# Optimization experiments

Measured on AMD Instinct MI355X. Metric: run time of the kernel, lower is better.

The kernel has to match this reference:

```python
import jax, jax.numpy as jnp
import numpy as np

B, C, H, W = 16, 3, 1024, 1024
OUT_HW = 224  # F.interpolate target size before the ResNet backbone
EPS = 1e-8


def setup_inputs() -> dict:
    key = jax.random.key(0)
    images = jax.random.uniform(key, (B, C, H, W), dtype=jnp.float32)
    return {"images": images}


def reference(images):
    # Batched FFT2 over spatial dims (replaces the per-(b,c) CPU numpy loop)
    fft = jnp.fft.fft2(images, axes=(-2, -1))                 # complex64 (B,C,H,W)
    fft = jnp.fft.fftshift(fft, axes=(-2, -1))
    spec = jnp.log1p(jnp.abs(fft))                             # log-magnitude spectrum

    # Per-sample min/max normalization to [0, 1] (flatten over C,H,W)
    b = spec.shape[0]
    flat = spec.reshape(b, -1)
    mn = flat.min(axis=1).reshape(b, 1, 1, 1)
    mx = flat.max(axis=1).reshape(b, 1, 1, 1)
    spec = (spec - mn) / (mx - mn + EPS)

    # Bilinear resize to 224x224; jax.image.resize 'bilinear' uses half-pixel
    # centers, matching torch F.interpolate(align_corners=False).
    out = jax.image.resize(spec, (b, spec.shape[1], OUT_HW, OUT_HW), method='bilinear')
    return out
```

## Files before the change

### kernel.cpp

```cpp
#include <hip/hip_runtime.h>
#include <math.h>

#define N 1024
#define BATCH 16
#define CH 3
#define BC 48
#define OUTHW 224
#define KSCALE (1024.0f / 224.0f)
#define SCALE  (224.0f / 1024.0f)
#define ABYTES ((size_t)BC * N * N * 8)
#define T1OFF  (768 * 2048)
#define SLOTOFF 1802240
#define WBAR() __builtin_amdgcn_wave_barrier()

#define CMUL(dr, di, ar, ai, br, bi) do {                         \
    float _r = (ar) * (br) - (ai) * (bi);                         \
    float _i = (ar) * (bi) + (ai) * (br);                         \
    (dr) = _r; (di) = _i; } while (0)

#define RADIX4(ar,ai,br,bi,cr,ci,dr,di, o0r,o0i,o1r,o1i,o2r,o2i,o3r,o3i) do { \
    float u0r=(ar)+(cr), u0i=(ai)+(ci);                           \
    float u1r=(ar)-(cr), u1i=(ai)-(ci);                           \
    float u2r=(br)+(dr), u2i=(bi)+(di);                           \
    float u3r=(bi)-(di), u3i=(dr)-(br);                           \
    (o0r)=u0r+u2r; (o0i)=u0i+u2i;                                 \
    (o1r)=u1r+u3r; (o1i)=u1i+u3i;                                 \
    (o2r)=u0r-u2r; (o2i)=u0i-u2i;                                 \
    (o3r)=u1r-u3r; (o3i)=u1i-u3i; } while (0)

__device__ __forceinline__ void dft16(float* xr, float* xi) {
  const float W16R[4][4] = {
    {1.f, 1.f, 1.f, 1.f},
    {1.f,  0.9238795325f,  0.7071067812f,  0.3826834324f},
    {1.f,  0.7071067812f,  0.0f,          -0.7071067812f},
    {1.f,  0.3826834324f, -0.7071067812f, -0.9238795325f}};
  const float W16I[4][4] = {
    {0.f, 0.f, 0.f, 0.f},
    {0.f, -0.3826834324f, -0.7071067812f, -0.9238795325f},
    {0.f, -0.7071067812f, -1.0f,          -0.7071067812f},
    {0.f, -0.9238795325f, -0.7071067812f,  0.3826834324f}};
  float tr[16], ti[16];
#pragma unroll
  for (int j = 0; j < 4; ++j) {
    RADIX4(xr[j],xi[j], xr[j+4],xi[j+4], xr[j+8],xi[j+8], xr[j+12],xi[j+12],
           tr[4*j],ti[4*j], tr[4*j+1],ti[4*j+1], tr[4*j+2],ti[4*j+2], tr[4*j+3],ti[4*j+3]);
  }
#pragma unroll
  for (int j = 0; j < 4; ++j) {
    float ar[4], ai_[4];
#pragma unroll
    for (int k = 0; k < 4; ++k) {
      if (j == 0 || k == 0) { ar[k] = tr[j+4*k]; ai_[k] = ti[j+4*k]; }
      else CMUL(ar[k], ai_[k], tr[j+4*k], ti[j+4*k], W16R[j][k], W16I[j][k]);
    }
    RADIX4(ar[0],ai_[0], ar[1],ai_[1], ar[2],ai_[2], ar[3],ai_[3],
           xr[j],xi[j], xr[j+4],xi[j+4], xr[j+8],xi[j+8], xr[j+12],xi[j+12]);
  }
}

__device__ __forceinline__ void stage2(float* xr, float* xi,
                                       const float2* __restrict__ twg, int j2) {
#pragma unroll
  for (int k = 1; k < 16; ++k) {
    float2 w = twg[4 * j2 * k];
    CMUL(xr[k], xi[k], xr[k], xi[k], w.x, w.y);
  }
  dft16(xr, xi);
}

__device__ __forceinline__ void wave_fft1024(float* xr, float* xi,
                                             float* sre, float* sim,
                                             const float2* __restrict__ twg, int l) {
  dft16(xr, xi);
#pragma unroll
  for (int k = 0; k < 16; ++k) { sre[17*l + k] = xr[k]; sim[17*l + k] = xi[k]; }
  WBAR();
  const int base2 = l + (l >> 4);
#pragma unroll
  for (int k = 0; k < 16; ++k) { xr[k] = sre[base2 + 68*k]; xi[k] = sim[base2 + 68*k]; }
  const int j2 = l & 15;
  stage2(xr, xi, twg, j2);
  const int ob = 272 * (l >> 4) + j2;
#pragma unroll
  for (int k = 0; k < 16; ++k) { sre[ob + 17*k] = xr[k]; sim[ob + 17*k] = xi[k]; }
  WBAR();
#pragma unroll
  for (int m = 0; m < 4; ++m) {
    float ar[4], ai_[4];
#pragma unroll
    for (int k = 0; k < 4; ++k) {
      ar[k] = sre[base2 + 68*m + 272*k];
      ai_[k] = sim[base2 + 68*m + 272*k];
    }
    const int j = l + 64*m;
#pragma unroll
    for (int k = 1; k < 4; ++k) {
      float2 w = twg[j * k];
      CMUL(ar[k], ai_[k], ar[k], ai_[k], w.x, w.y);
    }
    RADIX4(ar[0],ai_[0], ar[1],ai_[1], ar[2],ai_[2], ar[3],ai_[3],
           xr[m],xi[m], xr[m+4],xi[m+4], xr[m+8],xi[m+8], xr[m+12],xi[m+12]);
  }
}

__device__ __forceinline__ void wave_fft1024_1buf(float* xr, float* xi,
                                                  float* wb,
                                                  const float2* __restrict__ twg,
                                                  int l) {
  const int base2 = l + (l >> 4);
  const int j2 = l & 15;
  const int ob = 272 * (l >> 4) + j2;
  dft16(xr, xi);
#pragma unroll
  for (int k = 0; k < 16; ++k) wb[17*l + k] = xr[k];
  WBAR();
#pragma unroll
  for (int k = 0; k < 16; ++k) xr[k] = wb[base2 + 68*k];
  WBAR();
#pragma unroll
  for (int k = 0; k < 16; ++k) wb[17*l + k] = xi[k];
  WBAR();
#pragma unroll
  for (int k = 0; k < 16; ++k) xi[k] = wb[base2 + 68*k];
  WBAR();
  stage2(xr, xi, twg, j2);
#pragma unroll
  for (int k = 0; k < 16; ++k) wb[ob + 17*k] = xr[k];
  WBAR();
#pragma unroll
  for (int m = 0; m < 4; ++m)
#pragma unroll
    for (int k = 0; k < 4; ++k) xr[m + 4*k] = wb[base2 + 68*m + 272*k];
  WBAR();
#pragma unroll
  for (int k = 0; k < 16; ++k) wb[ob + 17*k] = xi[k];
  WBAR();
#pragma unroll
  for (int m = 0; m < 4; ++m)
#pragma unroll
    for (int k = 0; k < 4; ++k) xi[m + 4*k] = wb[base2 + 68*m + 272*k];
  WBAR();
#pragma unroll
  for (int m = 0; m < 4; ++m) {
    float ar[4], ai_[4];
#pragma unroll
    for (int k = 0; k < 4; ++k) { ar[k] = xr[m + 4*k]; ai_[k] = xi[m + 4*k]; }
    const int j = l + 64*m;
#pragma unroll
    for (int k = 1; k < 4; ++k) {
      float2 w = twg[j * k];
      CMUL(ar[k], ai_[k], ar[k], ai_[k], w.x, w.y);
    }
    RADIX4(ar[0],ai_[0], ar[1],ai_[1], ar[2],ai_[2], ar[3],ai_[3],
           xr[m],xi[m], xr[m+4],xi[m+4], xr[m+8],xi[m+8], xr[m+12],xi[m+12]);
  }
}

__global__ void k_init(float2* __restrict__ tw, int* __restrict__ slots) {
  int g = blockIdx.x * 256 + threadIdx.x;
  if (g < 1024) {
    float ang = -6.283185307179586f * ((float)g / 1024.0f);
    float s, c;
    sincosf(ang, &s, &c);
    tw[g] = make_float2(c, s);
    slots[g] = 0x7F800000;
  } else {
    slots[g] = 0;
  }
}

__global__ __launch_bounds__(256, 4) void k_rowfft(const float* __restrict__ in,
                                                   float2* __restrict__ A,
                                                   const float2* __restrict__ twg) {
  __shared__ float lds[8704];
  const int t  = threadIdx.x;
  const int w  = t >> 6;
  const int l  = t & 63;
  const int bc  = blockIdx.x >> 7;
  const int h0b = (blockIdx.x & 127) << 3;
  const int r0  = h0b + 2 * w;
  float* sre = lds + w * 2176;
  float* sim = sre + 1088;
  const float* row0 = in + ((size_t)bc << 20) + ((size_t)r0 << 10);
  const float* row1 = row0 + N;
  float xr[16], xi[16];
  const float sgn = (l & 1) ? -1.0f : 1.0f;
#pragma unroll
  for (int k = 0; k < 16; ++k) {
    xr[k] =  sgn * row0[l + 64*k];
    xi[k] = -sgn * row1[l + 64*k];
  }
  wave_fft1024(xr, xi, sre, sim, twg, l);
#pragma unroll
  for (int s = 0; s < 16; ++s) { sre[l + 64*s] = xr[s]; sim[l + 64*s] = xi[s]; }
  WBAR();
  float arr[9], ari[9], brr[9], bri[9];
#pragma unroll
  for (int s = 0; s < 9; ++s) {
    int i  = l + 64*s;
    int nk = (N - i) & (N - 1);
    float pr = xr[s], pi = xi[s];
    float qr = sre[nk], qi = sim[nk];
    arr[s] = 0.5f * (pr + qr); ari[s] = 0.5f * (pi - qi);
    brr[s] = 0.5f * (pi + qi); bri[s] = 0.5f * (qr - pr);
  }
  __syncthreads();
  float* stre = lds;
  float* stim = lds + 4160;
#pragma unroll
  for (int s = 0; s < 9; ++s) {
    int i = l + 64*s;
    if (i <= 512) {
      stre[(2*w)     * 520 + i] = arr[s]; stim[(2*w)     * 520 + i] = ari[s];
      stre[(2*w + 1) * 520 + i] = brr[s]; stim[(2*w + 1) * 520 + i] = bri[s];
    }
  }
  __syncthreads();
  const int rr = t & 7, v0 = t >> 3;
  float2* Abc = A + ((size_t)bc << 20);
#pragma unroll
  for (int i2 = 0; i2 < 17; ++i2) {
    int v = v0 + 32 * i2;
    if (v <= 512) {
      Abc[(size_t)v * N + h0b + rr] = make_float2(stre[rr*520 + v], stim[rr*520 + v]);
    }
  }
}

__global__ __launch_bounds__(256, 8) void k_colfft(const float2* __restrict__ A,
                                                   float* __restrict__ WSf,
                                                   int* __restrict__ slots,
                                                   const float2* __restrict__ twg) {
  __shared__ float lds[4352];
  const int t  = threadIdx.x;
  const int w  = t >> 6;
  const int l  = t & 63;
  const int gw = blockIdx.x * 4 + w;
  const int bc = gw / 513;
  const int sx = gw - bc * 513;
  const int b  = bc / CH;
  float* wb = lds + w * 1088;
  const float2* src = A + ((size_t)bc << 20) + ((size_t)sx << 10);
  float xr[16], xi[16];
#pragma unroll
  for (int k = 0; k < 16; ++k) { float2 v = src[l + 64*k]; xr[k] = v.x; xi[k] = v.y; }
  wave_fft1024_1buf(xr, xi, wb, twg, l);
  float lmin = 3.4e38f, lmax = 0.0f;
#pragma unroll
  for (int s = 0; s < 16; ++s) {
    float sp = __logf(1.0f + sqrtf(xr[s]*xr[s] + xi[s]*xi[s]));
    wb[l + 64*s] = sp;
    lmin = fminf(lmin, sp); lmax = fmaxf(lmax, sp);
  }
#pragma unroll
  for (int off = 32; off; off >>= 1) {
    lmin = fminf(lmin, __shfl_xor(lmin, off));
    lmax = fmaxf(lmax, __shfl_xor(lmax, off));
  }
  if (l == 0) {
    atomicMin(&slots[b * 64 + (sx & 63)],        __float_as_int(lmin));
    atomicMax(&slots[1024 + b * 64 + (sx & 63)], __float_as_int(lmax));
  }
  WBAR();
  float* T1 = WSf + ((size_t)bc << 21) + T1OFF;
  const bool mir = (sx != 0) && (sx != 512);
#pragma unroll
  for (int obk = 0; obk < 4; ++obk) {
    int oh = l + 64 * obk;
    if (oh < OUTHW) {
      float x = ((float)oh + 0.5f) * KSCALE - 0.5f;
      int jlo = (int)ceilf(x - KSCALE);
      float ssum = 0.0f, acc = 0.0f, accm = 0.0f;
#pragma unroll
      for (int u = 0; u < 10; ++u) {
        int j = jlo + u;
        float wgt = 1.0f - fabsf((float)j - x) * SCALE;
        wgt = fmaxf(wgt, 0.0f);
        bool valid = (j >= 0) && (j <= N - 1);
        if (!valid) wgt = 0.0f;
        int ja = valid ? j : 0;
        ssum += wgt;
        acc  += wgt * wb[ja];
        accm += wgt * wb[(N - ja) & (N - 1)];
      }
      float inv = 1.0f / ssum;
      T1[(size_t)sx * OUTHW + oh] = acc * inv;
      if (mir) T1[(size_t)(N - sx) * OUTHW + oh] = accm * inv;
    }
  }
}

__global__ __launch_bounds__(256) void k_resize2(const float2* __restrict__ A,
                                                 const int* __restrict__ slots,
                                                 float* __restrict__ out) {
  __shared__ float s2[2];
  const int ow = blockIdx.x % OUTHW;
  const int bc = blockIdx.x / OUTHW;
  const int b  = bc / CH;
  const int t  = threadIdx.x;
  if (t < 64) {
    int mn = slots[b * 64 + t];
#pragma unroll
    for (int off = 32; off; off >>= 1) mn = min(mn, __shfl_xor(mn, off));
    if (t == 0) s2[0] = __int_as_float(mn);
  } else if (t < 128) {
    int mx = slots[1024 + b * 64 + (t - 64)];
#pragma unroll
    for (int off = 32; off; off >>= 1) mx = max(mx, __shfl_xor(mx, off));
    if (t == 64) s2[1] = __int_as_float(mx);
  }
  __syncthreads();
  if (t >= OUTHW) return;
  const float mn = s2[0];
  const float mx = s2[1];
  const float inv = 1.0f / (mx - mn + 1e-8f);
  const float* T1 = (const float*)(A + ((size_t)bc << 20)) + T1OFF;
  float x = ((float)ow + 0.5f) * KSCALE - 0.5f;
  int jlo = (int)ceilf(x - KSCALE);
  float ssum = 0.0f, acc = 0.0f;
#pragma unroll
  for (int u = 0; u < 10; ++u) {
    int j = jlo + u;
    float wv = 1.0f - fabsf((float)j - x) * SCALE;
    wv = fmaxf(wv, 0.0f);
    bool valid = (j >= 0) && (j <= N - 1);
    if (!valid) wv = 0.0f;
    int ja = valid ? j : 0;
    ssum += wv;
    acc += wv * T1[(size_t)ja * OUTHW + t];
  }
  float v = acc / ssum;
  out[((size_t)bc * OUTHW + t) * OUTHW + ow] = (v - mn) * inv;
}

extern "C" void kernel_launch(void* const* d_in, const int* in_sizes, int n_in,
                              void* d_out, int out_size, void* d_ws, size_t ws_size,
                              hipStream_t stream) {
  const float* in = (const float*)d_in[0];
  float* out = (float*)d_out;
  float2* A = (float2*)d_ws;
  float* WSf = (float*)d_ws;
  float2* twg = (float2*)((char*)d_ws + ABYTES + 128);
  int* slots = (int*)(WSf + SLOTOFF);

  k_init<<<8, 256, 0, stream>>>(twg, slots);
  k_rowfft<<<BC * 128, 256, 0, stream>>>(in, A, twg);
  k_colfft<<<(BC * 513) / 4, 256, 0, stream>>>(A, WSf, slots, twg);
  k_resize2<<<BC * OUTHW, 256, 0, stream>>>(A, slots, out);
}
```

Baseline: 431.2 us.

## Widen row-FFT blocks to 16 rows with single-buffer LDS and split transposed store

The row-FFT kernel now runs 512-thread blocks that each handle 16 rows instead of 8. It switches to the single-buffer wave FFT, which stages real and imaginary parts through one LDS buffer per wave. The real/complex split and the transposed staging are done in two halves of the spectrum so that 16 rows fit in the same LDS. The goal is longer contiguous runs in the transposed global writes (16 consecutive complex values per column) and better occupancy. The cost is extra LDS round trips and barriers for the split passes.

```diff
diff --git a/kernel.cpp b/kernel.cpp
--- a/kernel.cpp
+++ b/kernel.cpp
@@ -68,41 +68,6 @@
   dft16(xr, xi);
 }
 
-__device__ __forceinline__ void wave_fft1024(float* xr, float* xi,
-                                             float* sre, float* sim,
-                                             const float2* __restrict__ twg, int l) {
-  dft16(xr, xi);
-#pragma unroll
-  for (int k = 0; k < 16; ++k) { sre[17*l + k] = xr[k]; sim[17*l + k] = xi[k]; }
-  WBAR();
-  const int base2 = l + (l >> 4);
-#pragma unroll
-  for (int k = 0; k < 16; ++k) { xr[k] = sre[base2 + 68*k]; xi[k] = sim[base2 + 68*k]; }
-  const int j2 = l & 15;
-  stage2(xr, xi, twg, j2);
-  const int ob = 272 * (l >> 4) + j2;
-#pragma unroll
-  for (int k = 0; k < 16; ++k) { sre[ob + 17*k] = xr[k]; sim[ob + 17*k] = xi[k]; }
-  WBAR();
-#pragma unroll
-  for (int m = 0; m < 4; ++m) {
-    float ar[4], ai_[4];
-#pragma unroll
-    for (int k = 0; k < 4; ++k) {
-      ar[k] = sre[base2 + 68*m + 272*k];
-      ai_[k] = sim[base2 + 68*m + 272*k];
-    }
-    const int j = l + 64*m;
-#pragma unroll
-    for (int k = 1; k < 4; ++k) {
-      float2 w = twg[j * k];
-      CMUL(ar[k], ai_[k], ar[k], ai_[k], w.x, w.y);
-    }
-    RADIX4(ar[0],ai_[0], ar[1],ai_[1], ar[2],ai_[2], ar[3],ai_[3],
-           xr[m],xi[m], xr[m+4],xi[m+4], xr[m+8],xi[m+8], xr[m+12],xi[m+12]);
-  }
-}
-
 __device__ __forceinline__ void wave_fft1024_1buf(float* xr, float* xi,
                                                   float* wb,
                                                   const float2* __restrict__ twg,
@@ -169,18 +134,17 @@
   }
 }
 
-__global__ __launch_bounds__(256, 4) void k_rowfft(const float* __restrict__ in,
+__global__ __launch_bounds__(512, 6) void k_rowfft(const float* __restrict__ in,
                                                    float2* __restrict__ A,
                                                    const float2* __restrict__ twg) {
   __shared__ float lds[8704];
   const int t  = threadIdx.x;
   const int w  = t >> 6;
   const int l  = t & 63;
-  const int bc  = blockIdx.x >> 7;
-  const int h0b = (blockIdx.x & 127) << 3;
+  const int bc  = blockIdx.x >> 6;
+  const int h0b = (blockIdx.x & 63) << 4;
   const int r0  = h0b + 2 * w;
-  float* sre = lds + w * 2176;
-  float* sim = sre + 1088;
+  float* wb = lds + w * 1088;
   const float* row0 = in + ((size_t)bc << 20) + ((size_t)r0 << 10);
   const float* row1 = row0 + N;
   float xr[16], xi[16];
@@ -190,39 +154,72 @@
     xr[k] =  sgn * row0[l + 64*k];
     xi[k] = -sgn * row1[l + 64*k];
   }
-  wave_fft1024(xr, xi, sre, sim, twg, l);
-#pragma unroll
-  for (int s = 0; s < 16; ++s) { sre[l + 64*s] = xr[s]; sim[l + 64*s] = xi[s]; }
-  WBAR();
-  float arr[9], ari[9], brr[9], bri[9];
-#pragma unroll
-  for (int s = 0; s < 9; ++s) {
-    int i  = l + 64*s;
-    int nk = (N - i) & (N - 1);
-    float pr = xr[s], pi = xi[s];
-    float qr = sre[nk], qi = sim[nk];
-    arr[s] = 0.5f * (pr + qr); ari[s] = 0.5f * (pi - qi);
-    brr[s] = 0.5f * (pi + qi); bri[s] = 0.5f * (qr - pr);
-  }
-  __syncthreads();
+  wave_fft1024_1buf(xr, xi, wb, twg, l);
   float* stre = lds;
   float* stim = lds + 4160;
-#pragma unroll
-  for (int s = 0; s < 9; ++s) {
-    int i = l + 64*s;
-    if (i <= 512) {
-      stre[(2*w)     * 520 + i] = arr[s]; stim[(2*w)     * 520 + i] = ari[s];
-      stre[(2*w + 1) * 520 + i] = brr[s]; stim[(2*w + 1) * 520 + i] = bri[s];
-    }
-  }
-  __syncthreads();
-  const int rr = t & 7, v0 = t >> 3;
+  const int rr = t & 15, v0 = t >> 4;
   float2* Abc = A + ((size_t)bc << 20);
 #pragma unroll
-  for (int i2 = 0; i2 < 17; ++i2) {
-    int v = v0 + 32 * i2;
-    if (v <= 512) {
-      Abc[(size_t)v * N + h0b + rr] = make_float2(stre[rr*520 + v], stim[rr*520 + v]);
+  for (int h = 0; h < 2; ++h) {
+    const int slo = (h == 0) ? 0 : 4;
+    const int cnt = (h == 0) ? 4 : 5;
+    float par[5], pai[5], pbr[5], pbi[5];
+    __syncthreads();
+#pragma unroll
+    for (int s = 0; s < 16; ++s) wb[l + 64*s] = xr[s];
+    WBAR();
+#pragma unroll
+    for (int u = 0; u < 5; ++u) {
+      if (u < cnt) {
+        int s = slo + u;
+        int i = l + 64*s;
+        if (i <= 512) {
+          float qr = wb[(N - i) & (N - 1)];
+          par[u] = 0.5f * (xr[s] + qr);
+          pbi[u] = 0.5f * (qr - xr[s]);
+        }
+      }
+    }
+    WBAR();
+#pragma unroll
+    for (int s = 0; s < 16; ++s) wb[l + 64*s] = xi[s];
+    WBAR();
+#pragma unroll
+    for (int u = 0; u < 5; ++u) {
+      if (u < cnt) {
+        int s = slo + u;
+        int i = l + 64*s;
+        if (i <= 512) {
+          float qi = wb[(N - i) & (N - 1)];
+          pai[u] = 0.5f * (xi[s] - qi);
+          pbr[u] = 0.5f * (xi[s] + qi);
+        }
+      }
+    }
+    __syncthreads();
+#pragma unroll
+    for (int u = 0; u < 5; ++u) {
+      if (u < cnt) {
+        int s = slo + u;
+        int i = l + 64*s;
+        if (i <= 512) {
+          int c = i - 256 * h;
+          stre[(2*w)     * 260 + c] = par[u]; stim[(2*w)     * 260 + c] = pai[u];
+          stre[(2*w + 1) * 260 + c] = pbr[u]; stim[(2*w + 1) * 260 + c] = pbi[u];
+        }
+      }
+    }
+    __syncthreads();
+#pragma unroll
+    for (int i2 = 0; i2 < 9; ++i2) {
+      if (i2 < 8 + h) {
+        int v = 256 * h + v0 + 32 * i2;
+        if (v <= 512) {
+          int c = v - 256 * h;
+          Abc[(size_t)v * N + h0b + rr] =
+              make_float2(stre[rr*260 + c], stim[rr*260 + c]);
+        }
+      }
     }
   }
 }
@@ -344,7 +341,7 @@
   int* slots = (int*)(WSf + SLOTOFF);
 
   k_init<<<8, 256, 0, stream>>>(twg, slots);
-  k_rowfft<<<BC * 128, 256, 0, stream>>>(in, A, twg);
+  k_rowfft<<<BC * 64, 512, 0, stream>>>(in, A, twg);
   k_colfft<<<(BC * 513) / 4, 256, 0, stream>>>(A, WSf, slots, twg);
   k_resize2<<<BC * OUTHW, 256, 0, stream>>>(A, slots, out);
 }
```

Result: no change. 431.9 us (+0.2%).
